# Kernel tuning notes

Hardware: AMD Instinct MI355X
Metric: run time of the kernel (lower is better)

## Reference

```python
import jax, jax.numpy as jnp
import numpy as np

SIZES = jnp.array([128.0, 256.0, 512.0], dtype=jnp.float32)
RATIOS = jnp.array([0.5, 1.0, 2.0], dtype=jnp.float32)
SCORE_THR = 0.05
IOU_THR = 0.7
MIN_SIZE = 16.0
MAX_PROP = 1000
PRE_NMS = 1000


def _base_anchors():
    # torchvision-style base anchors: (x1,y1,x2,y2) centered at origin, rounded
    h_r = jnp.sqrt(RATIOS)
    w_r = 1.0 / h_r
    ws = (w_r[:, None] * SIZES[None, :]).reshape(-1)  # (9,)
    hs = (h_r[:, None] * SIZES[None, :]).reshape(-1)
    return jnp.round(jnp.stack([-ws, -hs, ws, hs], axis=1) / 2.0)  # (9,4)


def _grid_anchors(img_h, img_w, fh, fw):
    # stride = image_size // feature_size; anchors ordered (y, x, anchor)
    sh, sw = img_h // fh, img_w // fw
    sx = jnp.arange(fw, dtype=jnp.float32) * sw
    sy = jnp.arange(fh, dtype=jnp.float32) * sh
    yy, xx = jnp.meshgrid(sy, sx, indexing='ij')
    xf = xx.reshape(-1)
    yf = yy.reshape(-1)
    shifts = jnp.stack([xf, yf, xf, yf], axis=1)  # (H*W, 4)
    return (shifts[:, None, :] + _base_anchors()[None, :, :]).reshape(-1, 4)  # (H*W*9, 4)


def _conv(x, w, b, pad):
    y = jax.lax.conv_general_dilated(x, w, (1, 1), pad,
                                     dimension_numbers=('NCHW', 'OIHW', 'NCHW'))
    return y + b[None, :, None, None]


def _bbox_adjust(anchors, deltas):
    # anchors, deltas: (..., 4); deltas = (dx, dy, dw, dh)
    aw = anchors[..., 2] - anchors[..., 0]
    ah = anchors[..., 3] - anchors[..., 1]
    cx = anchors[..., 0] + 0.5 * aw
    cy = anchors[..., 1] + 0.5 * ah
    ncx = deltas[..., 0] * aw + cx
    ncy = deltas[..., 1] * ah + cy
    nw = jnp.exp(deltas[..., 2]) * aw
    nh = jnp.exp(deltas[..., 3]) * ah
    return jnp.stack([ncx - 0.5 * nw, ncy - 0.5 * nh,
                      ncx + 0.5 * nw, ncy + 0.5 * nh], axis=-1)


def _pairwise_iou(b):
    area = (b[:, 2] - b[:, 0]) * (b[:, 3] - b[:, 1])
    lt = jnp.maximum(b[:, None, :2], b[None, :, :2])
    rb = jnp.minimum(b[:, None, 2:], b[None, :, 2:])
    wh = jnp.clip(rb - lt, 0.0)
    inter = wh[..., 0] * wh[..., 1]
    return inter / (area[:, None] + area[None, :] - inter + 1e-8)


def _per_image(boxes, scores, img_h, img_w):
    # clip to image, filter small / low-score, greedy NMS, pad to MAX_PROP
    x1 = jnp.clip(boxes[:, 0], 0.0, img_w)
    y1 = jnp.clip(boxes[:, 1], 0.0, img_h)
    x2 = jnp.clip(boxes[:, 2], 0.0, img_w)
    y2 = jnp.clip(boxes[:, 3], 0.0, img_h)
    b = jnp.stack([x1, y1, x2, y2], axis=1)
    valid = ((x2 - x1) >= MIN_SIZE) & ((y2 - y1) >= MIN_SIZE) & (scores > SCORE_THR)
    s = jnp.where(valid, scores, -1.0)
    topv, topi = jax.lax.top_k(s, PRE_NMS)
    tb = b[topi]  # (PRE_NMS, 4) sorted by score desc
    iou = _pairwise_iou(tb)
    idx = jnp.arange(PRE_NMS)

    def body(i, keep):
        sup = (iou[i] > IOU_THR) & keep[i] & (idx > i)
        return keep & ~sup

    keep = jax.lax.fori_loop(0, PRE_NMS, body, jnp.ones(PRE_NMS, dtype=bool))
    s2 = jnp.where(keep & (topv > 0.0), topv, -1.0)
    fv, fi = jax.lax.top_k(s2, MAX_PROP)
    return jnp.where((fv > 0.0)[:, None], tb[fi], 0.0)  # (MAX_PROP, 4)


def _forward(image_list, feature_map, conv_w, conv_b, cls_w, cls_b, bbox_w, bbox_b):
    N, C, H, W = feature_map.shape
    img_h, img_w = image_list.shape[2], image_list.shape[3]
    out = _conv(feature_map, conv_w, conv_b, 'SAME')  # (N, mid, H, W)
    # faithful to original: cls reshaped directly (no permute), bbox permuted
    cls = jax.nn.sigmoid(_conv(out, cls_w, cls_b, 'VALID')).reshape(N, -1, 2)
    bb = _conv(out, bbox_w, bbox_b, 'VALID').transpose(0, 2, 3, 1).reshape(N, -1, 4)
    anchors = _grid_anchors(img_h, img_w, H, W)  # (H*W*9, 4)
    dec = _bbox_adjust(anchors[None], bb)        # (N, M, 4)
    scores = cls[:, :, 1]                        # objectness
    fh, fw = float(img_h), float(img_w)
    fb = jax.vmap(lambda bx, sc: _per_image(bx, sc, fh, fw))(dec, scores)  # (N, MAX_PROP, 4)
    roi = fb.reshape(-1, 4)
    bidx = jnp.repeat(jnp.arange(N, dtype=roi.dtype), MAX_PROP)[:, None]
    return jnp.concatenate([roi, bidx], axis=1)  # (N*MAX_PROP, 5)


def setup_inputs() -> dict:
    key = jax.random.key(0)
    ks = jax.random.split(key, 6)
    image_list = jax.random.normal(ks[0], (8, 3, 800, 800), dtype=jnp.float32)
    feature_map = jax.random.normal(ks[1], (8, 512, 50, 50), dtype=jnp.float32)
    conv_w = 0.02 * jax.random.normal(ks[2], (256, 512, 3, 3), dtype=jnp.float32)
    conv_b = jnp.zeros((256,), dtype=jnp.float32)
    cls_w = 0.02 * jax.random.normal(ks[3], (18, 256, 1, 1), dtype=jnp.float32)
    cls_b = jnp.zeros((18,), dtype=jnp.float32)
    bbox_w = 0.01 * jax.random.normal(ks[4], (36, 256, 1, 1), dtype=jnp.float32)
    bbox_b = jnp.zeros((36,), dtype=jnp.float32)
    return {"image_list": image_list, "feature_map": feature_map,
            "conv_w": conv_w, "conv_b": conv_b, "cls_w": cls_w, "cls_b": cls_b,
            "bbox_w": bbox_w, "bbox_b": bbox_b}


def reference(image_list, feature_map, conv_w, conv_b, cls_w, cls_b, bbox_w, bbox_b):
    return _forward(image_list, feature_map, conv_w, conv_b, cls_w, cls_b, bbox_w, bbox_b)
```

## Files before the change

kernel.cpp:

```cpp
#include <hip/hip_runtime.h>
#include <cstdint>

#define N_IMG 8
#define CIN 512
#define COUT 256
#define FH 50
#define FW 50
#define SPAT 2500
#define NANCH 22500
#define KTOP 1000
#define PART_ELEMS 5120000

__global__ __launch_bounds__(256) void k_conv3_part(const float* __restrict__ in,
                                                    const float* __restrict__ w,
                                                    double* __restrict__ parts,
                                                    int S)
{
    __shared__ double ind[2][1152];

    const int tile = blockIdx.x, ocg = blockIdx.y;
    const int n = blockIdx.z / S, s = blockIdx.z - n * S;
    const int ccp = 64 / S;
    const int cc0 = s * ccp, cc1 = cc0 + ccp;
    const int ty = tile / 5, tx = tile % 5;
    const int y0 = ty * 10, x0 = tx * 10;
    const int t = threadIdx.x;
    const int oc_l = t & 63;
    const int g = t >> 6;
    const int base_ly = (g >> 1) * 5, base_lx = (g & 1) * 5;
    const int oc0 = ocg * 64;

    int soff[5];
#pragma unroll
    for (int k = 0; k < 5; k++) {
        int idx = t + k * 256;
        soff[k] = -1;
        if (idx < 1152) {
            int c = idx / 144, rem = idx - c * 144;
            int iy = rem / 12, ix = rem - iy * 12;
            int y = y0 - 1 + iy, x = x0 - 1 + ix;
            if ((unsigned)y < 50u && (unsigned)x < 50u)
                soff[k] = (n * CIN + c) * SPAT + y * FW + x;
        }
    }

    const float* wrow = w + (size_t)(oc0 + oc_l) * (CIN * 9);

    double acc[5][5];
#pragma unroll
    for (int i = 0; i < 5; i++)
#pragma unroll
        for (int j = 0; j < 5; j++) acc[i][j] = 0.0;

    float rin[5];
    {
        const int coff0 = cc0 * (8 * SPAT);
#pragma unroll
        for (int k = 0; k < 5; k++) rin[k] = (soff[k] >= 0) ? in[soff[k] + coff0] : 0.0f;
    }
    float wnxt[9];
    {
        const float* wp0 = wrow + cc0 * 72;
#pragma unroll
        for (int k = 0; k < 9; k++) wnxt[k] = wp0[k];
    }

    for (int cc = cc0; cc < cc1; ++cc) {
        const int cur = cc & 1;
#pragma unroll
        for (int k = 0; k < 5; k++) {
            int idx = t + k * 256;
            if (idx < 1152) ind[cur][idx] = (double)rin[k];
        }
        __syncthreads();

        if (cc + 1 < cc1) {
            const int coff = (cc + 1) * (8 * SPAT);
#pragma unroll
            for (int k = 0; k < 5; k++)
                rin[k] = (soff[k] >= 0) ? in[soff[k] + coff] : 0.0f;
        }

#pragma unroll 1
        for (int c = 0; c < 8; c++) {
            double wd[9];
#pragma unroll
            for (int k = 0; k < 9; k++) wd[k] = (double)wnxt[k];
            const int nidx = cc * 8 + c + 1;
            if (nidx < cc1 * 8) {
                const float* wp = wrow + nidx * 9;
#pragma unroll
                for (int k = 0; k < 9; k++) wnxt[k] = wp[k];
            }
#pragma unroll
            for (int r = 0; r < 7; r++) {
                double drow[7];
#pragma unroll
                for (int j = 0; j < 7; j++)
                    drow[j] = ind[cur][c * 144 + (base_ly + r) * 12 + base_lx + j];
#pragma unroll
                for (int dy = 0; dy < 3; dy++) {
                    const int iy = r - dy;
                    if (iy >= 0 && iy < 5) {
#pragma unroll
                        for (int dx = 0; dx < 3; dx++) {
                            const double wdv = wd[dy * 3 + dx];
#pragma unroll
                            for (int ix = 0; ix < 5; ix++)
                                acc[iy][ix] = fma(wdv, drow[ix + dx], acc[iy][ix]);
                        }
                    }
                }
            }
        }
        __syncthreads();
    }

    double* po = parts + (size_t)s * PART_ELEMS + (size_t)(n * COUT + oc0 + oc_l) * SPAT;
#pragma unroll
    for (int iy = 0; iy < 5; iy++)
#pragma unroll
        for (int ix = 0; ix < 5; ix++)
            po[(y0 + base_ly + iy) * FW + (x0 + base_lx + ix)] = acc[iy][ix];
}

__global__ __launch_bounds__(256) void k_heads_fused(const double* __restrict__ parts,
                                                     int S,
                                                     const float* __restrict__ conv_b,
                                                     const float* __restrict__ cls_w,
                                                     const float* __restrict__ cls_b,
                                                     const float* __restrict__ bbox_w,
                                                     const float* __restrict__ bbox_b,
                                                     double* __restrict__ boxesd,
                                                     double* __restrict__ scored)
{
    __shared__ float feat[25 * 257];
    __shared__ double outb[54 * 25];
    const int blk = blockIdx.x, n = blockIdx.y;
    const int pos0 = blk * 25;
    const int t = threadIdx.x;

    for (int idx = t; idx < 6400; idx += 256) {
        int c = idx / 25, p = idx - c * 25;
        size_t base = (size_t)(n * COUT + c) * SPAT + pos0 + p;
        double a = parts[base];
        for (int sp = 1; sp < S; sp++) a += parts[(size_t)sp * PART_ELEMS + base];
        a += (double)conv_b[c];
        feat[p * 257 + c] = (float)a;
    }
    __syncthreads();

    for (int u = t; u < 1350; u += 256) {
        const int oc = u % 54, p = u / 54;
        const float* wp = (oc < 18) ? (cls_w + oc * COUT) : (bbox_w + (oc - 18) * COUT);
        double s = (double)((oc < 18) ? cls_b[oc] : bbox_b[oc - 18]);
        const float* fp = &feat[p * 257];
#pragma unroll 8
        for (int c = 0; c < COUT; c++) s = fma((double)wp[c], (double)fp[c], s);
        outb[oc * 25 + p] = s;
    }
    __syncthreads();

    if (t < 225) {
        const int p = t / 9, k = t - p * 9;
        const int pos = pos0 + p;
        const int y = pos / 50, x = pos - y * 50;
        const int ri = k / 3, si = k - ri * 3;
        const double ratio = (ri == 0) ? 0.5 : ((ri == 1) ? 1.0 : 2.0);
        const double size = (si == 0) ? 128.0 : ((si == 1) ? 256.0 : 512.0);
        const double hr = sqrt(ratio), wr = 1.0 / hr;
        const double wsz = wr * size, hsz = hr * size;
        const double bx0 = rint(-wsz * 0.5), by0 = rint(-hsz * 0.5);
        const double bx1 = rint(wsz * 0.5), by1 = rint(hsz * 0.5);
        const double sxf = (double)(x * 16), syf = (double)(y * 16);
        const double a0 = sxf + bx0, a1 = syf + by0, a2 = sxf + bx1, a3 = syf + by1;
        const double aw = a2 - a0, ah = a3 - a1;
        const double cx = a0 + 0.5 * aw, cy = a1 + 0.5 * ah;
        const double d0 = outb[(18 + k * 4 + 0) * 25 + p];
        const double d1 = outb[(18 + k * 4 + 1) * 25 + p];
        const double d2 = outb[(18 + k * 4 + 2) * 25 + p];
        const double d3 = outb[(18 + k * 4 + 3) * 25 + p];
        const double ncx = d0 * aw + cx, ncy = d1 * ah + cy;
        const double nw = exp(d2) * aw, nh = exp(d3) * ah;
        double x1 = ncx - 0.5 * nw, y1 = ncy - 0.5 * nh;
        double x2 = ncx + 0.5 * nw, y2 = ncy + 0.5 * nh;
        x1 = fmin(fmax(x1, 0.0), 800.0);
        y1 = fmin(fmax(y1, 0.0), 800.0);
        x2 = fmin(fmax(x2, 0.0), 800.0);
        y2 = fmin(fmax(y2, 0.0), 800.0);
        double* bp = boxesd + ((size_t)n * NANCH + pos * 9 + k) * 4;
        bp[0] = x1; bp[1] = y1; bp[2] = x2; bp[3] = y2;
    }
    for (int u = t; u < 450; u += 256) {
        const int ch = u / 25, p = u - ch * 25;
        const int pos = pos0 + p;
        if (pos & 1) {
            const int a = ch * 1250 + ((pos - 1) >> 1);
            const double v = outb[ch * 25 + p];
            scored[(size_t)n * NANCH + a] = 1.0 / (1.0 + exp(-v));
        }
    }
}

__global__ __launch_bounds__(128) void k_conv3_full(const float* __restrict__ in,
                                                    const float* __restrict__ w,
                                                    const float* __restrict__ bias,
                                                    float* __restrict__ out)
{
    __shared__ double ind[2][672];
    const int tile = blockIdx.x, ocg = blockIdx.y, n = blockIdx.z;
    const int ty = tile / 5, tx = tile % 5;
    const int y0 = ty * 5, x0 = tx * 10;
    const int t = threadIdx.x;
    const int oc_l = t & 63;
    const int g = t >> 6;
    const int base_lx = g * 5;
    const int oc0 = ocg * 64;

    int soff[6];
#pragma unroll
    for (int k = 0; k < 6; k++) {
        int idx = t + k * 128;
        soff[k] = -1;
        if (idx < 672) {
            int c = idx / 84, rem = idx - c * 84;
            int iy = rem / 12, ix = rem - iy * 12;
            int y = y0 - 1 + iy, x = x0 - 1 + ix;
            if ((unsigned)y < 50u && (unsigned)x < 50u)
                soff[k] = (n * CIN + c) * SPAT + y * FW + x;
        }
    }
    const float* wrow = w + (size_t)(oc0 + oc_l) * (CIN * 9);
    double acc[5][5];
#pragma unroll
    for (int i = 0; i < 5; i++)
#pragma unroll
        for (int j = 0; j < 5; j++) acc[i][j] = 0.0;
    float rin[6];
#pragma unroll
    for (int k = 0; k < 6; k++) rin[k] = (soff[k] >= 0) ? in[soff[k]] : 0.0f;
    float wnxt[9];
#pragma unroll
    for (int k = 0; k < 9; k++) wnxt[k] = wrow[k];

    for (int cc = 0; cc < 64; ++cc) {
        const int cur = cc & 1;
#pragma unroll
        for (int k = 0; k < 6; k++) {
            int idx = t + k * 128;
            if (idx < 672) ind[cur][idx] = (double)rin[k];
        }
        __syncthreads();
        if (cc < 63) {
            const int coff = (cc + 1) * (8 * SPAT);
#pragma unroll
            for (int k = 0; k < 6; k++)
                rin[k] = (soff[k] >= 0) ? in[soff[k] + coff] : 0.0f;
        }
#pragma unroll 1
        for (int c = 0; c < 8; c++) {
            double wd[9];
#pragma unroll
            for (int k = 0; k < 9; k++) wd[k] = (double)wnxt[k];
            const int nidx = cc * 8 + c + 1;
            if (nidx < 512) {
                const float* wp = wrow + nidx * 9;
#pragma unroll
                for (int k = 0; k < 9; k++) wnxt[k] = wp[k];
            }
#pragma unroll
            for (int r = 0; r < 7; r++) {
                double drow[7];
#pragma unroll
                for (int j = 0; j < 7; j++)
                    drow[j] = ind[cur][c * 84 + r * 12 + base_lx + j];
#pragma unroll
                for (int dy = 0; dy < 3; dy++) {
                    const int iy = r - dy;
                    if (iy >= 0 && iy < 5) {
#pragma unroll
                        for (int dx = 0; dx < 3; dx++) {
                            const double wdv = wd[dy * 3 + dx];
#pragma unroll
                            for (int ix = 0; ix < 5; ix++)
                                acc[iy][ix] = fma(wdv, drow[ix + dx], acc[iy][ix]);
                        }
                    }
                }
            }
        }
        __syncthreads();
    }
    const double b = (double)bias[oc0 + oc_l];
#pragma unroll
    for (int iy = 0; iy < 5; iy++)
#pragma unroll
        for (int ix = 0; ix < 5; ix++) {
            int y = y0 + iy, x = x0 + base_lx + ix;
            out[(n * COUT + oc0 + oc_l) * SPAT + y * FW + x] = (float)(acc[iy][ix] + b);
        }
}

__global__ __launch_bounds__(256) void k_heads_legacy(const float* __restrict__ conv1,
                                                      const float* __restrict__ cls_w,
                                                      const float* __restrict__ cls_b,
                                                      const float* __restrict__ bbox_w,
                                                      const float* __restrict__ bbox_b,
                                                      double* __restrict__ boxesd,
                                                      double* __restrict__ scored)
{
    __shared__ float feat[25 * 257];
    __shared__ double outb[54 * 25];
    const int blk = blockIdx.x, n = blockIdx.y;
    const int pos0 = blk * 25;
    const int t = threadIdx.x;

    for (int idx = t; idx < 6400; idx += 256) {
        int c = idx / 25, p = idx - c * 25;
        feat[p * 257 + c] = conv1[(n * COUT + c) * SPAT + pos0 + p];
    }
    __syncthreads();
    for (int u = t; u < 1350; u += 256) {
        const int oc = u % 54, p = u / 54;
        const float* wp = (oc < 18) ? (cls_w + oc * COUT) : (bbox_w + (oc - 18) * COUT);
        double s = (double)((oc < 18) ? cls_b[oc] : bbox_b[oc - 18]);
        const float* fp = &feat[p * 257];
#pragma unroll 8
        for (int c = 0; c < COUT; c++) s = fma((double)wp[c], (double)fp[c], s);
        outb[oc * 25 + p] = s;
    }
    __syncthreads();
    if (t < 225) {
        const int p = t / 9, k = t - p * 9;
        const int pos = pos0 + p;
        const int y = pos / 50, x = pos - y * 50;
        const int ri = k / 3, si = k - ri * 3;
        const double ratio = (ri == 0) ? 0.5 : ((ri == 1) ? 1.0 : 2.0);
        const double size = (si == 0) ? 128.0 : ((si == 1) ? 256.0 : 512.0);
        const double hr = sqrt(ratio), wr = 1.0 / hr;
        const double wsz = wr * size, hsz = hr * size;
        const double bx0 = rint(-wsz * 0.5), by0 = rint(-hsz * 0.5);
        const double bx1 = rint(wsz * 0.5), by1 = rint(hsz * 0.5);
        const double sxf = (double)(x * 16), syf = (double)(y * 16);
        const double a0 = sxf + bx0, a1 = syf + by0, a2 = sxf + bx1, a3 = syf + by1;
        const double aw = a2 - a0, ah = a3 - a1;
        const double cx = a0 + 0.5 * aw, cy = a1 + 0.5 * ah;
        const double d0 = outb[(18 + k * 4 + 0) * 25 + p];
        const double d1 = outb[(18 + k * 4 + 1) * 25 + p];
        const double d2 = outb[(18 + k * 4 + 2) * 25 + p];
        const double d3 = outb[(18 + k * 4 + 3) * 25 + p];
        const double ncx = d0 * aw + cx, ncy = d1 * ah + cy;
        const double nw = exp(d2) * aw, nh = exp(d3) * ah;
        double x1 = ncx - 0.5 * nw, y1 = ncy - 0.5 * nh;
        double x2 = ncx + 0.5 * nw, y2 = ncy + 0.5 * nh;
        x1 = fmin(fmax(x1, 0.0), 800.0);
        y1 = fmin(fmax(y1, 0.0), 800.0);
        x2 = fmin(fmax(x2, 0.0), 800.0);
        y2 = fmin(fmax(y2, 0.0), 800.0);
        double* bp = boxesd + ((size_t)n * NANCH + pos * 9 + k) * 4;
        bp[0] = x1; bp[1] = y1; bp[2] = x2; bp[3] = y2;
    }
    for (int u = t; u < 450; u += 256) {
        const int ch = u / 25, p = u - ch * 25;
        const int pos = pos0 + p;
        if (pos & 1) {
            const int a = ch * 1250 + ((pos - 1) >> 1);
            const double v = outb[ch * 25 + p];
            scored[(size_t)n * NANCH + a] = 1.0 / (1.0 + exp(-v));
        }
    }
}

__global__ __launch_bounds__(1024) void k_select(const double* __restrict__ boxesd,
                                                 const double* __restrict__ scored,
                                                 uint64_t* __restrict__ keys,
                                                 double* __restrict__ tbd,
                                                 float* __restrict__ topv)
{
    __shared__ unsigned hist[256];
    __shared__ uint64_t selk[1024];
    __shared__ uint32_t seli[1024];
    __shared__ uint64_t sh_prefix, sh_mask;
    __shared__ unsigned sh_rem, sh_cntA, sh_cntB;

    const int n = blockIdx.x, t = threadIdx.x;
    uint64_t* ky = keys + (size_t)n * NANCH;

    for (int a = t; a < NANCH; a += 1024) {
        const double* bp = boxesd + ((size_t)n * NANCH + a) * 4;
        double x1 = bp[0], y1 = bp[1], x2 = bp[2], y2 = bp[3];
        double s0 = scored[(size_t)n * NANCH + a];
        bool valid = (x2 - x1 >= 16.0) && (y2 - y1 >= 16.0) && (s0 > 0.05);
        double s = valid ? s0 : -1.0;
        uint64_t b = (uint64_t)__double_as_longlong(s);
        uint64_t su = (b >> 63) ? ~b : (b | 0x8000000000000000ull);
        ky[a] = su;
    }
    if (t == 0) { sh_prefix = 0; sh_mask = 0; sh_rem = KTOP; }
    __syncthreads();

    for (int pass = 0; pass < 8; pass++) {
        const int shift = 56 - 8 * pass;
        if (t < 256) hist[t] = 0;
        __syncthreads();
        const uint64_t pre = sh_prefix, msk = sh_mask;
        for (int a = t; a < NANCH; a += 1024) {
            uint64_t k = ky[a];
            if ((k & msk) == pre)
                atomicAdd(&hist[(unsigned)((k >> shift) & 255)], 1u);
        }
        __syncthreads();
        if (t == 0) {
            unsigned rem = sh_rem;
            int v = 255;
            for (; v > 0; v--) {
                unsigned c = hist[v];
                if (rem <= c) break;
                rem -= c;
            }
            sh_prefix = pre | ((uint64_t)(unsigned)v << shift);
            sh_mask = msk | (255ull << shift);
            sh_rem = rem;
        }
        __syncthreads();
    }
    const uint64_t T = sh_prefix;
    selk[t] = 0; seli[t] = 0xFFFFFFFFu;
    if (t == 0) { sh_cntA = 0; sh_cntB = 0; }
    __syncthreads();
    for (int a = t; a < NANCH; a += 1024) {
        uint64_t k = ky[a];
        if (k > T) {
            unsigned p = atomicAdd(&sh_cntA, 1u);
            selk[p] = k; seli[p] = (uint32_t)a;
        }
    }
    __syncthreads();
    const unsigned m = sh_cntA;
    for (int a = t; a < NANCH; a += 1024) {
        uint64_t k = ky[a];
        if (k == T) {
            unsigned q = atomicAdd(&sh_cntB, 1u);
            unsigned slot = m + q;
            if (slot < KTOP) { selk[slot] = k; seli[slot] = (uint32_t)a; }
        }
    }
    __syncthreads();
    for (int k2 = 2; k2 <= 1024; k2 <<= 1) {
        for (int j = k2 >> 1; j > 0; j >>= 1) {
            int ixj = t ^ j;
            if (ixj > t) {
                bool asc = ((t & k2) == 0);
                uint64_t ka = selk[t], kb = selk[ixj];
                uint32_t ia = seli[t], ib = seli[ixj];
                bool gt = (ka > kb) || (ka == kb && ia < ib);
                if (gt == asc) { selk[t] = kb; selk[ixj] = ka; seli[t] = ib; seli[ixj] = ia; }
            }
            __syncthreads();
        }
    }
    if (t < KTOP) {
        uint64_t k = selk[1023 - t];
        uint32_t idx = seli[1023 - t];
        uint64_t b = (k >> 63) ? (k ^ 0x8000000000000000ull) : ~k;
        double s = __longlong_as_double((long long)b);
        const double* bp = boxesd + ((size_t)n * NANCH + idx) * 4;
        double* tp = tbd + ((size_t)n * KTOP + t) * 4;
        tp[0] = bp[0]; tp[1] = bp[1]; tp[2] = bp[2]; tp[3] = bp[3];
        topv[n * KTOP + t] = (float)s;
    }
}

__global__ __launch_bounds__(256) void k_supmat(const double* __restrict__ tbd,
                                                uint64_t* __restrict__ sup)
{
    __shared__ double sb[4000];
    const int tile = blockIdx.x, n = blockIdx.y;
    const int t = threadIdx.x;
    for (int i = t; i < 4000; i += 256) sb[i] = tbd[(size_t)n * KTOP * 4 + i];
    __syncthreads();
    const int r0 = tile * 64;
    for (int u = t; u < 1024; u += 256) {
        const int il = u >> 4, wq = u & 15;
        const int i = r0 + il;
        if (i >= 1000) continue;
        const double bix = sb[i * 4], biy = sb[i * 4 + 1], biz = sb[i * 4 + 2], biw = sb[i * 4 + 3];
        const double ai = (biz - bix) * (biw - biy);
        uint64_t bits = 0;
        const int jbase = wq * 64;
        for (int jj = 0; jj < 64; jj++) {
            const int j = jbase + jj;
            if (j < 1000 && j > i) {
                const double bjx = sb[j * 4], bjy = sb[j * 4 + 1], bjz = sb[j * 4 + 2], bjw = sb[j * 4 + 3];
                const double aj = (bjz - bjx) * (bjw - bjy);
                const double ltx = fmax(bix, bjx), lty = fmax(biy, bjy);
                const double rbx = fmin(biz, bjz), rby = fmin(biw, bjw);
                const double ww = fmax(rbx - ltx, 0.0), hh = fmax(rby - lty, 0.0);
                const double inter = ww * hh;
                const double iou = inter / (ai + aj - inter + 1e-8);
                if (iou > 0.7) bits |= (1ull << jj);
            }
        }
        sup[((size_t)n * KTOP + i) * 16 + wq] = bits;
    }
}

__global__ __launch_bounds__(64) void k_nms(const uint64_t* __restrict__ sup,
                                            uint64_t* __restrict__ keepout)
{
    const int n = blockIdx.x;
    const int lane = threadIdx.x;
    const uint64_t* rows = sup + (size_t)n * KTOP * 16;

    uint64_t keep;
    if (lane < 15) keep = ~0ull;
    else if (lane == 15) keep = (1ull << 40) - 1;
    else keep = 0;

    uint64_t A[8], B[8];
    auto LOADG = [&](uint64_t* dst, int g) {
#pragma unroll
        for (int k = 0; k < 8; k++) {
            int i = g * 8 + k;
            dst[k] = (lane < 16) ? rows[(size_t)i * 16 + lane] : 0ull;
        }
    };
    auto PROCG = [&](const uint64_t* src, int g) {
#pragma unroll
        for (int k = 0; k < 8; k++) {
            int i = g * 8 + k;
            uint64_t kw = __shfl(keep, i >> 6);
            bool alive = (kw >> (i & 63)) & 1ull;
            keep &= alive ? ~src[k] : ~0ull;
        }
    };

    LOADG(A, 0);
    for (int g = 0; g < 125; g += 2) {
        if (g + 1 < 125) LOADG(B, g + 1);
        PROCG(A, g);
        if (g + 2 < 125) LOADG(A, g + 2);
        if (g + 1 < 125) PROCG(B, g + 1);
    }
    if (lane < 16) keepout[n * 16 + lane] = keep;
}

__global__ __launch_bounds__(1024) void k_final(const uint64_t* __restrict__ keepw,
                                                const float* __restrict__ topv,
                                                const double* __restrict__ tbd,
                                                float* __restrict__ out)
{
    __shared__ int sc[1024];
    __shared__ uint64_t kw[16];
    __shared__ int sh_total;
    const int n = blockIdx.x, t = threadIdx.x;
    if (t < 16) kw[t] = keepw[n * 16 + t];
    __syncthreads();

    int val = 0;
    bool kept = false;
    if (t < 1000) {
        bool bit = (kw[t >> 6] >> (t & 63)) & 1ull;
        float v = topv[n * KTOP + t];
        kept = bit && (v > 0.0f);
        val = kept ? 1 : 0;
    }
    sc[t] = val;
    __syncthreads();
    for (int off = 1; off < 1024; off <<= 1) {
        int x = (t >= off) ? sc[t - off] : 0;
        __syncthreads();
        sc[t] += x;
        __syncthreads();
    }
    if (t == 1023) sh_total = sc[1023];
    __syncthreads();
    const int total = sh_total;
    if (t < 1000) {
        if (kept) {
            int r = sc[t] - 1;
            const double* bp = tbd + ((size_t)n * KTOP + t) * 4;
            float* o = out + ((size_t)n * KTOP + r) * 5;
            o[0] = (float)bp[0]; o[1] = (float)bp[1];
            o[2] = (float)bp[2]; o[3] = (float)bp[3];
            o[4] = (float)n;
        }
        if (t >= total) {
            float* o = out + ((size_t)n * KTOP + t) * 5;
            o[0] = 0.0f; o[1] = 0.0f; o[2] = 0.0f; o[3] = 0.0f; o[4] = (float)n;
        }
    }
}

extern "C" void kernel_launch(void* const* d_in, const int* in_sizes, int n_in,
                              void* d_out, int out_size, void* d_ws, size_t ws_size,
                              hipStream_t stream)
{
    (void)in_sizes; (void)n_in; (void)out_size;
    const float* feat   = (const float*)d_in[1];
    const float* conv_w = (const float*)d_in[2];
    const float* conv_b = (const float*)d_in[3];
    const float* cls_w  = (const float*)d_in[4];
    const float* cls_b  = (const float*)d_in[5];
    const float* bbox_w = (const float*)d_in[6];
    const float* bbox_b = (const float*)d_in[7];
    float* out = (float*)d_out;
    char* ws = (char*)d_ws;

    const size_t PB   = 40960000ull;
    const size_t REST = 5760000 + 1440000 + 1440000 + 256000 + 32000 + 1024000 + 1024;

    int S = 0;
    if      (ws_size >= 4 * PB + REST) S = 4;
    else if (ws_size >= 2 * PB + REST) S = 2;
    else if (ws_size >= 1 * PB + REST) S = 1;

    if (S > 0) {
        double*   parts  = (double*)ws;
        char*     p      = ws + (size_t)S * PB;
        double*   boxesd = (double*)(p);               p += 5760000;
        double*   scored = (double*)(p);               p += 1440000;
        uint64_t* keys   = (uint64_t*)(p);             p += 1440000;
        double*   tbd    = (double*)(p);               p += 256000;
        float*    topv   = (float*)(p);                p += 32000;
        uint64_t* sup    = (uint64_t*)(p);             p += 1024000;
        uint64_t* keepw  = (uint64_t*)(p);

        k_conv3_part <<<dim3(25, 4, 8 * S), 256, 0, stream>>>(feat, conv_w, parts, S);
        k_heads_fused<<<dim3(100, 8), 256, 0, stream>>>(parts, S, conv_b, cls_w, cls_b,
                                                        bbox_w, bbox_b, boxesd, scored);
        k_select<<<8, 1024, 0, stream>>>(boxesd, scored, keys, tbd, topv);
        k_supmat<<<dim3(16, 8), 256, 0, stream>>>(tbd, sup);
        k_nms   <<<8, 64, 0, stream>>>(sup, keepw);
        k_final <<<8, 1024, 0, stream>>>(keepw, topv, tbd, out);
    } else {
        float*    conv1  = (float*)(ws);
        double*   boxesd = (double*)(ws + 20480000);
        double*   scored = (double*)(ws + 26240000);
        uint64_t* keys   = (uint64_t*)(ws + 27680000);
        double*   tbd    = (double*)(ws + 29120000);
        float*    topv   = (float*)(ws + 29376000);
        uint64_t* sup    = (uint64_t*)(ws + 29408000);
        uint64_t* keepw  = (uint64_t*)(ws + 30432000);

        k_conv3_full  <<<dim3(50, 4, 8), 128, 0, stream>>>(feat, conv_w, conv_b, conv1);
        k_heads_legacy<<<dim3(100, 8), 256, 0, stream>>>(conv1, cls_w, cls_b, bbox_w, bbox_b, boxesd, scored);
        k_select<<<8, 1024, 0, stream>>>(boxesd, scored, keys, tbd, topv);
        k_supmat<<<dim3(16, 8), 256, 0, stream>>>(tbd, sup);
        k_nms   <<<8, 64, 0, stream>>>(sup, keepw);
        k_final <<<8, 1024, 0, stream>>>(keepw, topv, tbd, out);
    }
}
```

Baseline: 1.500 ms.

## Widen conv blocks to 128 channels, add split-K 8, rework top-k selection

The 3x3 conv kernel now uses 512 threads covering 128 output channels per block, so each staged input tile is reused across twice as many channels, and a split-K factor of 8 is allowed when the workspace is large enough. In k_select, the first two radix passes use wave-aggregated histogram atomics, the serial threshold scan becomes a parallel shuffle scan, and the bitonic sort is replaced by an O(n^2) rank-by-counting sort over packed key/index pairs. Padding entries are now explicitly marked invalid. Risks include higher register pressure at 512 threads, more partial-sum traffic in the heads kernel with S=8, and 1024 shared-memory reads per thread in the rank sort.

```diff
diff --git a/kernel.cpp b/kernel.cpp
--- a/kernel.cpp
+++ b/kernel.cpp
@@ -11,7 +11,7 @@
 #define KTOP 1000
 #define PART_ELEMS 5120000
 
-__global__ __launch_bounds__(256) void k_conv3_part(const float* __restrict__ in,
+__global__ __launch_bounds__(512) void k_conv3_part(const float* __restrict__ in,
                                                     const float* __restrict__ w,
                                                     double* __restrict__ parts,
                                                     int S)
@@ -25,15 +25,15 @@
     const int ty = tile / 5, tx = tile % 5;
     const int y0 = ty * 10, x0 = tx * 10;
     const int t = threadIdx.x;
-    const int oc_l = t & 63;
-    const int g = t >> 6;
+    const int oc_l = t & 127;
+    const int g = t >> 7;
     const int base_ly = (g >> 1) * 5, base_lx = (g & 1) * 5;
-    const int oc0 = ocg * 64;
-
-    int soff[5];
-#pragma unroll
-    for (int k = 0; k < 5; k++) {
-        int idx = t + k * 256;
+    const int oc0 = ocg * 128;
+
+    int soff[3];
+#pragma unroll
+    for (int k = 0; k < 3; k++) {
+        int idx = t + k * 512;
         soff[k] = -1;
         if (idx < 1152) {
             int c = idx / 144, rem = idx - c * 144;
@@ -52,11 +52,11 @@
 #pragma unroll
         for (int j = 0; j < 5; j++) acc[i][j] = 0.0;
 
-    float rin[5];
+    float rin[3];
     {
         const int coff0 = cc0 * (8 * SPAT);
 #pragma unroll
-        for (int k = 0; k < 5; k++) rin[k] = (soff[k] >= 0) ? in[soff[k] + coff0] : 0.0f;
+        for (int k = 0; k < 3; k++) rin[k] = (soff[k] >= 0) ? in[soff[k] + coff0] : 0.0f;
     }
     float wnxt[9];
     {
@@ -68,8 +68,8 @@
     for (int cc = cc0; cc < cc1; ++cc) {
         const int cur = cc & 1;
 #pragma unroll
-        for (int k = 0; k < 5; k++) {
-            int idx = t + k * 256;
+        for (int k = 0; k < 3; k++) {
+            int idx = t + k * 512;
             if (idx < 1152) ind[cur][idx] = (double)rin[k];
         }
         __syncthreads();
@@ -77,7 +77,7 @@
         if (cc + 1 < cc1) {
             const int coff = (cc + 1) * (8 * SPAT);
 #pragma unroll
-            for (int k = 0; k < 5; k++)
+            for (int k = 0; k < 3; k++)
                 rin[k] = (soff[k] >= 0) ? in[soff[k] + coff] : 0.0f;
         }
 
@@ -378,8 +378,8 @@
                                                  float* __restrict__ topv)
 {
     __shared__ unsigned hist[256];
-    __shared__ uint64_t selk[1024];
-    __shared__ uint32_t seli[1024];
+    __shared__ __align__(16) uint64_t sel2[2048];
+    __shared__ __align__(16) uint64_t out2[2048];
     __shared__ uint64_t sh_prefix, sh_mask;
     __shared__ unsigned sh_rem, sh_cntA, sh_cntB;
 
@@ -404,35 +404,74 @@
         if (t < 256) hist[t] = 0;
         __syncthreads();
         const uint64_t pre = sh_prefix, msk = sh_mask;
-        for (int a = t; a < NANCH; a += 1024) {
-            uint64_t k = ky[a];
-            if ((k & msk) == pre)
-                atomicAdd(&hist[(unsigned)((k >> shift) & 255)], 1u);
-        }
-        __syncthreads();
-        if (t == 0) {
-            unsigned rem = sh_rem;
-            int v = 255;
-            for (; v > 0; v--) {
-                unsigned c = hist[v];
-                if (rem <= c) break;
-                rem -= c;
-            }
-            sh_prefix = pre | ((uint64_t)(unsigned)v << shift);
-            sh_mask = msk | (255ull << shift);
-            sh_rem = rem;
+        if (pass < 2) {
+            for (int a = t; a < NANCH; a += 1024) {
+                uint64_t k = ky[a];
+                bool p = ((k & msk) == pre);
+                unsigned d = (unsigned)((k >> shift) & 255);
+                unsigned long long todo = __ballot(p);
+                while (todo) {
+                    int leader = __ffsll((unsigned long long)todo) - 1;
+                    unsigned dl = __shfl(d, leader);
+                    unsigned long long mm = __ballot(p && (d == dl));
+                    if ((t & 63) == leader)
+                        atomicAdd(&hist[dl], (unsigned)__popcll(mm));
+                    todo &= ~mm;
+                }
+            }
+        } else {
+            for (int a = t; a < NANCH; a += 1024) {
+                uint64_t k = ky[a];
+                if ((k & msk) == pre)
+                    atomicAdd(&hist[(unsigned)((k >> shift) & 255)], 1u);
+            }
+        }
+        __syncthreads();
+        if (t < 64) {
+            unsigned h0 = hist[4 * t], h1 = hist[4 * t + 1];
+            unsigned h2 = hist[4 * t + 2], h3 = hist[4 * t + 3];
+            unsigned local = h0 + h1 + h2 + h3;
+            unsigned suf = local;
+#pragma unroll
+            for (int off = 1; off < 64; off <<= 1) {
+                unsigned x = __shfl_down(suf, off);
+                if (t + off < 64) suf += x;
+            }
+            unsigned exclc = suf - local;
+            unsigned inc3 = exclc + h3;
+            unsigned inc2 = inc3 + h2;
+            unsigned inc1 = inc2 + h1;
+            unsigned inc0 = inc1 + h0;
+            const unsigned rem = sh_rem;
+            int cand = -1; unsigned candExcl = 0;
+            if      (inc3 >= rem) { cand = 4 * t + 3; candExcl = exclc; }
+            else if (inc2 >= rem) { cand = 4 * t + 2; candExcl = inc3; }
+            else if (inc1 >= rem) { cand = 4 * t + 1; candExcl = inc2; }
+            else if (inc0 >= rem) { cand = 4 * t + 0; candExcl = inc1; }
+#pragma unroll
+            for (int off = 32; off > 0; off >>= 1) {
+                int c2 = __shfl_down(cand, off);
+                unsigned p2 = __shfl_down(candExcl, off);
+                if (c2 > cand) { cand = c2; candExcl = p2; }
+            }
+            if (t == 0) {
+                sh_prefix = pre | ((uint64_t)(unsigned)cand << shift);
+                sh_mask = msk | (255ull << shift);
+                sh_rem = rem - candExcl;
+            }
         }
         __syncthreads();
     }
     const uint64_t T = sh_prefix;
-    selk[t] = 0; seli[t] = 0xFFFFFFFFu;
+
+    sel2[2 * t] = 0; sel2[2 * t + 1] = 0;
     if (t == 0) { sh_cntA = 0; sh_cntB = 0; }
     __syncthreads();
     for (int a = t; a < NANCH; a += 1024) {
         uint64_t k = ky[a];
         if (k > T) {
             unsigned p = atomicAdd(&sh_cntA, 1u);
-            selk[p] = k; seli[p] = (uint32_t)a;
+            sel2[2 * p] = k; sel2[2 * p + 1] = (uint64_t)(~(uint32_t)a);
         }
     }
     __syncthreads();
@@ -442,32 +481,39 @@
         if (k == T) {
             unsigned q = atomicAdd(&sh_cntB, 1u);
             unsigned slot = m + q;
-            if (slot < KTOP) { selk[slot] = k; seli[slot] = (uint32_t)a; }
-        }
-    }
-    __syncthreads();
-    for (int k2 = 2; k2 <= 1024; k2 <<= 1) {
-        for (int j = k2 >> 1; j > 0; j >>= 1) {
-            int ixj = t ^ j;
-            if (ixj > t) {
-                bool asc = ((t & k2) == 0);
-                uint64_t ka = selk[t], kb = selk[ixj];
-                uint32_t ia = seli[t], ib = seli[ixj];
-                bool gt = (ka > kb) || (ka == kb && ia < ib);
-                if (gt == asc) { selk[t] = kb; selk[ixj] = ka; seli[t] = ib; seli[ixj] = ia; }
-            }
-            __syncthreads();
-        }
-    }
+            if (slot < KTOP) { sel2[2 * slot] = k; sel2[2 * slot + 1] = (uint64_t)(~(uint32_t)a); }
+        }
+    }
+    __syncthreads();
+    {
+        const uint64_t myk = sel2[2 * t], myn = sel2[2 * t + 1];
+        int rank = 0;
+        const ulonglong2* sp = (const ulonglong2*)sel2;
+#pragma unroll 8
+        for (int j = 0; j < 1024; j++) {
+            ulonglong2 v = sp[j];
+            rank += (v.x > myk) || (v.x == myk && v.y > myn);
+        }
+        if (rank < KTOP) { out2[2 * rank] = myk; out2[2 * rank + 1] = myn; }
+    }
+    __syncthreads();
+
     if (t < KTOP) {
-        uint64_t k = selk[1023 - t];
-        uint32_t idx = seli[1023 - t];
+        uint64_t k = out2[2 * t];
+        uint32_t idx = ~(uint32_t)out2[2 * t + 1];
         uint64_t b = (k >> 63) ? (k ^ 0x8000000000000000ull) : ~k;
         double s = __longlong_as_double((long long)b);
-        const double* bp = boxesd + ((size_t)n * NANCH + idx) * 4;
+        double bx0 = 0.0, bx1 = 0.0, bx2 = 0.0, bx3 = 0.0;
+        float sv = (float)s;
+        if (idx < NANCH) {
+            const double* bp = boxesd + ((size_t)n * NANCH + idx) * 4;
+            bx0 = bp[0]; bx1 = bp[1]; bx2 = bp[2]; bx3 = bp[3];
+        } else {
+            sv = -1.0f;
+        }
         double* tp = tbd + ((size_t)n * KTOP + t) * 4;
-        tp[0] = bp[0]; tp[1] = bp[1]; tp[2] = bp[2]; tp[3] = bp[3];
-        topv[n * KTOP + t] = (float)s;
+        tp[0] = bx0; tp[1] = bx1; tp[2] = bx2; tp[3] = bx3;
+        topv[n * KTOP + t] = sv;
     }
 }
 
@@ -611,7 +657,8 @@
     const size_t REST = 5760000 + 1440000 + 1440000 + 256000 + 32000 + 1024000 + 1024;
 
     int S = 0;
-    if      (ws_size >= 4 * PB + REST) S = 4;
+    if      (ws_size >= 8 * PB + REST) S = 8;
+    else if (ws_size >= 4 * PB + REST) S = 4;
     else if (ws_size >= 2 * PB + REST) S = 2;
     else if (ws_size >= 1 * PB + REST) S = 1;
 
@@ -626,7 +673,7 @@
         uint64_t* sup    = (uint64_t*)(p);             p += 1024000;
         uint64_t* keepw  = (uint64_t*)(p);
 
-        k_conv3_part <<<dim3(25, 4, 8 * S), 256, 0, stream>>>(feat, conv_w, parts, S);
+        k_conv3_part <<<dim3(25, 2, 8 * S), 512, 0, stream>>>(feat, conv_w, parts, S);
         k_heads_fused<<<dim3(100, 8), 256, 0, stream>>>(parts, S, conv_b, cls_w, cls_b,
                                                         bbox_w, bbox_b, boxesd, scored);
         k_select<<<8, 1024, 0, stream>>>(boxesd, scored, keys, tbd, topv);
```

Result: slower. 1.646 ms (+9.8%).
